# Performance work log

Hardware: AMD Instinct MI355X
Metric: run time of the kernel (lower is better)

Reference implementation:

```python
import jax, jax.numpy as jnp
import numpy as np
import math

D = 1024
H = 16
DH = D // H
B, M, N = 4, 1024, 2048
LN_EPS = 1e-5


def setup_inputs() -> dict:
    key = jax.random.key(0)
    ks = jax.random.split(key, 8)
    s = 1.0 / math.sqrt(D)  # keep logits well-scaled
    return {
        "Q": jax.random.normal(ks[0], (B, M, D), jnp.float32),
        "KV": jax.random.normal(ks[1], (B, N, D), jnp.float32),
        "log_gate_bias": jax.random.normal(ks[2], (B, N), jnp.float32),
        "Wq": jax.random.normal(ks[3], (D, D), jnp.float32) * s,
        "bq": jnp.zeros((D,), jnp.float32),
        "Wk": jax.random.normal(ks[4], (D, D), jnp.float32) * s,
        "bk": jnp.zeros((D,), jnp.float32),
        "Wv": jax.random.normal(ks[5], (D, D), jnp.float32) * s,
        "bv": jnp.zeros((D,), jnp.float32),
        "Wo": jax.random.normal(ks[6], (D, D), jnp.float32) * s,
        "bo": jnp.zeros((D,), jnp.float32),
        "gamma": jnp.ones((D,), jnp.float32),
        "beta": jnp.zeros((D,), jnp.float32),
    }


def reference(Q, KV, log_gate_bias, Wq, bq, Wk, bk, Wv, bv, Wo, bo, gamma, beta):
    b, m, d = Q.shape
    n = KV.shape[1]
    # projections (torch Linear: x @ W.T + b), split heads -> (b, h, len, dh)
    q = (Q @ Wq.T + bq).reshape(b, m, H, DH).transpose(0, 2, 1, 3)
    k = (KV @ Wk.T + bk).reshape(b, n, H, DH).transpose(0, 2, 1, 3)
    v = (KV @ Wv.T + bv).reshape(b, n, H, DH).transpose(0, 2, 1, 3)
    scores = jnp.einsum('bhmd,bhnd->bhmn', q, k) / math.sqrt(DH)
    # additive gate bias broadcast over heads and queries: (b,1,1,n)
    scores = scores + log_gate_bias[:, None, None, :]
    attn = jax.nn.softmax(scores, axis=-1)
    out = jnp.einsum('bhmn,bhnd->bhmd', attn, v)
    out = out.transpose(0, 2, 1, 3).reshape(b, m, d)
    out = out @ Wo.T + bo
    # dropout p=0.0 (eval) -> identity; residual + LayerNorm
    x = Q + out
    mu = jnp.mean(x, axis=-1, keepdims=True)
    var = jnp.mean(jnp.square(x - mu), axis=-1, keepdims=True)
    return gamma * (x - mu) * jax.lax.rsqrt(var + LN_EPS) + beta
```

## Files before the change

kernel.cpp:

```cpp
#include <hip/hip_runtime.h>
#include <hip/hip_bf16.h>

#define DMODEL 1024
#define NHEAD  16
#define DHEAD  64
#define BB     4
#define MM     1024
#define NN     2048
#define LOG2E  1.4426950408889634f

typedef __attribute__((ext_vector_type(8))) short bf16x8;
typedef __attribute__((ext_vector_type(4))) float f32x4;

#define AS1 __attribute__((address_space(1)))
#define AS3 __attribute__((address_space(3)))

__device__ __forceinline__ unsigned short f2bf(float f) {
  unsigned int u = __builtin_bit_cast(unsigned int, f);
  unsigned int r = (u + 0x7fffu + ((u >> 16) & 1u)) >> 16;
  return (unsigned short)r;
}

__global__ __launch_bounds__(256)
void cast_all(const float* __restrict__ Q, const float* __restrict__ KV,
              const float* __restrict__ W0, const float* __restrict__ W1,
              const float* __restrict__ W2, const float* __restrict__ W3,
              unsigned short* __restrict__ oQ, unsigned short* __restrict__ oKV,
              unsigned short* __restrict__ o0, unsigned short* __restrict__ o1,
              unsigned short* __restrict__ o2, unsigned short* __restrict__ o3)
{
  const int bid = blockIdx.x;
  const float* s; unsigned short* d; int i;
  if (bid < 4096)       { s = Q;  d = oQ;  i = bid * 256 + threadIdx.x; }
  else if (bid < 12288) { s = KV; d = oKV; i = (bid - 4096) * 256 + threadIdx.x; }
  else {
    const int w = (bid - 12288) >> 10;
    s = w == 0 ? W0 : w == 1 ? W1 : w == 2 ? W2 : W3;
    d = w == 0 ? o0 : w == 1 ? o1 : w == 2 ? o2 : o3;
    i = ((bid - 12288) & 1023) * 256 + threadIdx.x;
  }
  const float4 v = ((const float4*)s)[i];
  union { unsigned short us[4]; unsigned long long u64; } o;
  o.us[0] = f2bf(v.x); o.us[1] = f2bf(v.y); o.us[2] = f2bf(v.z); o.us[3] = f2bf(v.w);
  *(unsigned long long*)(d + (size_t)i * 4) = o.u64;
}

__global__ __launch_bounds__(256)
void qkv_gemm(const unsigned short* __restrict__ Qbf,
              const unsigned short* __restrict__ KVbf,
              const unsigned short* __restrict__ Wqb,
              const unsigned short* __restrict__ Wkb,
              const unsigned short* __restrict__ Wvb,
              const float* __restrict__ bq, const float* __restrict__ bk,
              const float* __restrict__ bv,
              unsigned short* __restrict__ qout,
              unsigned short* __restrict__ kout,
              unsigned short* __restrict__ vtout)
{
  __shared__ unsigned short As[3][128 * 32];
  __shared__ unsigned short Ws[3][128 * 32];

  const int bid = blockIdx.x;
  const unsigned short* A; const unsigned short* W; const float* bias;
  int mode, lb, nmb;
  if (bid < 256)      { A = Qbf;  W = Wqb; bias = bq; mode = 0; lb = bid;       nmb = 4; }
  else if (bid < 768) { A = KVbf; W = Wkb; bias = bk; mode = 1; lb = bid - 256; nmb = 8; }
  else                { A = KVbf; W = Wvb; bias = bv; mode = 2; lb = bid - 768; nmb = 8; }
  const int xcd = lb & 7;
  const int l   = lb >> 3;
  const int mb  = xcd * nmb + (l >> 3);
  const int nb  = l & 7;

  const int tid  = threadIdx.x;
  const int wave = tid >> 6;
  const int lane = tid & 63;
  const int l15  = lane & 15;
  const int l4   = lane >> 4;
  const int wm   = wave >> 1;
  const int wn   = wave & 1;
  const size_t row0 = (size_t)mb * 128;
  const size_t col0 = (size_t)nb * 128;

  f32x4 acc[4][4] = {};

  const int cc0 = (wave * 2) * 64 + lane;
  const int cc1 = cc0 + 64;
  const int r0 = cc0 >> 2, sch0 = (cc0 & 3) ^ (r0 & 3);
  const int r1 = cc1 >> 2, sch1 = (cc1 & 3) ^ (r1 & 3);
  const unsigned short* ap0 = A + (row0 + r0) * DMODEL + sch0 * 8;
  const unsigned short* ap1 = A + (row0 + r1) * DMODEL + sch1 * 8;
  const unsigned short* wp0 = W + (col0 + r0) * DMODEL + sch0 * 8;
  const unsigned short* wp1 = W + (col0 + r1) * DMODEL + sch1 * 8;

  auto stage = [&](int buf) {
    __builtin_amdgcn_global_load_lds((const AS1 void*)ap0, (AS3 void*)(&As[buf][cc0 * 8]), 16, 0, 0);
    __builtin_amdgcn_global_load_lds((const AS1 void*)ap1, (AS3 void*)(&As[buf][cc1 * 8]), 16, 0, 0);
    __builtin_amdgcn_global_load_lds((const AS1 void*)wp0, (AS3 void*)(&Ws[buf][cc0 * 8]), 16, 0, 0);
    __builtin_amdgcn_global_load_lds((const AS1 void*)wp1, (AS3 void*)(&Ws[buf][cc1 * 8]), 16, 0, 0);
    ap0 += 32; ap1 += 32; wp0 += 32; wp1 += 32;
  };

  stage(0);
  stage(1);

  int cur = 0;
  for (int kt = 0; kt < 32; ++kt) {
    if (kt < 31) {
      asm volatile("s_waitcnt vmcnt(4)" ::: "memory");
    } else {
      asm volatile("s_waitcnt vmcnt(0)" ::: "memory");
    }
    __builtin_amdgcn_sched_barrier(0);
    __builtin_amdgcn_s_barrier();
    __builtin_amdgcn_sched_barrier(0);
    if (kt < 30) {
      int nxt = cur + 2; if (nxt >= 3) nxt -= 3;
      stage(nxt);
    }

    bf16x8 af[4], bfr[4];
#pragma unroll
    for (int mi = 0; mi < 4; ++mi) {
      int r = wm * 64 + mi * 16 + l15;
      af[mi] = *(const bf16x8*)&As[cur][r * 32 + ((l4 ^ (r & 3)) << 3)];
    }
#pragma unroll
    for (int ni = 0; ni < 4; ++ni) {
      int r = wn * 64 + ni * 16 + l15;
      bfr[ni] = *(const bf16x8*)&Ws[cur][r * 32 + ((l4 ^ (r & 3)) << 3)];
    }
    __builtin_amdgcn_s_setprio(1);
#pragma unroll
    for (int mi = 0; mi < 4; ++mi)
#pragma unroll
      for (int ni = 0; ni < 4; ++ni)
        acc[mi][ni] = __builtin_amdgcn_mfma_f32_16x16x32_bf16(af[mi], bfr[ni], acc[mi][ni], 0, 0, 0);
    __builtin_amdgcn_s_setprio(0);

    cur = (cur == 2) ? 0 : cur + 1;
  }

#pragma unroll
  for (int mi = 0; mi < 4; ++mi) {
#pragma unroll
    for (int ni = 0; ni < 4; ++ni) {
      const int col = (int)col0 + wn * 64 + ni * 16 + l15;
      const float bcol = bias[col];
      if (mode == 2) {
        const int row = (int)row0 + wm * 64 + mi * 16 + l4 * 4;
        const int b = row >> 11, n = row & 2047;
        const int h = col >> 6, d = col & 63;
        union { unsigned short us[4]; uint2 u; } pk;
#pragma unroll
        for (int i = 0; i < 4; ++i)
          pk.us[i] = __builtin_bit_cast(unsigned short, __float2bfloat16(acc[mi][ni][i] + bcol));
        *(uint2*)(vtout + (((size_t)(b * 16 + h) * 64 + d) << 11) + n) = pk.u;
      } else {
#pragma unroll
        for (int i = 0; i < 4; ++i) {
          const size_t row = row0 + wm * 64 + mi * 16 + l4 * 4 + i;
          float v = acc[mi][ni][i] + bcol;
          if (mode == 0) v *= (0.125f * LOG2E);
          (mode == 0 ? qout : kout)[row * DMODEL + col] =
            __builtin_bit_cast(unsigned short, __float2bfloat16(v));
        }
      }
    }
  }
}

__global__ __launch_bounds__(256)
void gemm_o(const unsigned short* __restrict__ A,
            const unsigned short* __restrict__ W,
            const float* __restrict__ bias,
            const float* __restrict__ resid,
            float* __restrict__ out)
{
  __shared__ unsigned short As[3][64 * 32];
  __shared__ unsigned short Ws[3][128 * 32];

  const int bid = blockIdx.x;
  const int xcd = bid & 7;
  const int l   = bid >> 3;
  const int mb  = xcd * 8 + (l >> 3);
  const int nb  = l & 7;

  const int tid  = threadIdx.x;
  const int wave = tid >> 6;
  const int lane = tid & 63;
  const int l15  = lane & 15;
  const int l4   = lane >> 4;
  const int wm   = wave >> 1;
  const int wn   = wave & 1;
  const size_t row0 = (size_t)mb * 64;
  const size_t col0 = (size_t)nb * 128;

  f32x4 acc[2][4] = {};

  const int ra = tid >> 2, scha = (tid & 3) ^ (ra & 3);
  const int cc0 = (wave * 2) * 64 + lane;
  const int cc1 = cc0 + 64;
  const int r0 = cc0 >> 2, sch0 = (cc0 & 3) ^ (r0 & 3);
  const int r1 = cc1 >> 2, sch1 = (cc1 & 3) ^ (r1 & 3);
  const unsigned short* ap  = A + (row0 + ra) * DMODEL + scha * 8;
  const unsigned short* wp0 = W + (col0 + r0) * DMODEL + sch0 * 8;
  const unsigned short* wp1 = W + (col0 + r1) * DMODEL + sch1 * 8;

  auto stage = [&](int buf) {
    __builtin_amdgcn_global_load_lds((const AS1 void*)ap,  (AS3 void*)(&As[buf][tid * 8]), 16, 0, 0);
    __builtin_amdgcn_global_load_lds((const AS1 void*)wp0, (AS3 void*)(&Ws[buf][cc0 * 8]), 16, 0, 0);
    __builtin_amdgcn_global_load_lds((const AS1 void*)wp1, (AS3 void*)(&Ws[buf][cc1 * 8]), 16, 0, 0);
    ap += 32; wp0 += 32; wp1 += 32;
  };

  stage(0);
  stage(1);

  int cur = 0;
  for (int kt = 0; kt < 32; ++kt) {
    if (kt < 31) {
      asm volatile("s_waitcnt vmcnt(3)" ::: "memory");
    } else {
      asm volatile("s_waitcnt vmcnt(0)" ::: "memory");
    }
    __builtin_amdgcn_sched_barrier(0);
    __builtin_amdgcn_s_barrier();
    __builtin_amdgcn_sched_barrier(0);
    if (kt < 30) {
      int nxt = cur + 2; if (nxt >= 3) nxt -= 3;
      stage(nxt);
    }

    bf16x8 af[2], bfr[4];
#pragma unroll
    for (int mi = 0; mi < 2; ++mi) {
      int r = wm * 32 + mi * 16 + l15;
      af[mi] = *(const bf16x8*)&As[cur][r * 32 + ((l4 ^ (r & 3)) << 3)];
    }
#pragma unroll
    for (int ni = 0; ni < 4; ++ni) {
      int r = wn * 64 + ni * 16 + l15;
      bfr[ni] = *(const bf16x8*)&Ws[cur][r * 32 + ((l4 ^ (r & 3)) << 3)];
    }
    __builtin_amdgcn_s_setprio(1);
#pragma unroll
    for (int mi = 0; mi < 2; ++mi)
#pragma unroll
      for (int ni = 0; ni < 4; ++ni)
        acc[mi][ni] = __builtin_amdgcn_mfma_f32_16x16x32_bf16(af[mi], bfr[ni], acc[mi][ni], 0, 0, 0);
    __builtin_amdgcn_s_setprio(0);

    cur = (cur == 2) ? 0 : cur + 1;
  }

#pragma unroll
  for (int mi = 0; mi < 2; ++mi) {
#pragma unroll
    for (int ni = 0; ni < 4; ++ni) {
      const int col = (int)col0 + wn * 64 + ni * 16 + l15;
      const float bcol = bias[col];
#pragma unroll
      for (int i = 0; i < 4; ++i) {
        const size_t row = row0 + wm * 32 + mi * 16 + l4 * 4 + i;
        const size_t idx = row * DMODEL + col;
        out[idx] = resid[idx] + acc[mi][ni][i] + bcol;
      }
    }
  }
}

__global__ __launch_bounds__(512, 4)
void attn_kernel(const unsigned short* __restrict__ qb,
                 const unsigned short* __restrict__ kb,
                 const unsigned short* __restrict__ vt,
                 const float* __restrict__ lgb,
                 unsigned short* __restrict__ attn)
{
  __shared__ unsigned short Ks[2][64 * 64];
  __shared__ unsigned short Vs[2][64 * 64];
  __shared__ float Gs[2][64];
  __shared__ unsigned short Ps[8][16 * 64];

  const int tid  = threadIdx.x;
  const int wave = tid >> 6;
  const int lane = tid & 63;
  const int l15  = lane & 15;
  const int l4   = lane >> 4;

  const int bid  = blockIdx.x;
  const int xcd  = bid & 7;
  const int slot = bid >> 3;
  const int m_i  = slot & 7;
  const int grp  = slot >> 3;
  const int bh   = grp * 8 + xcd;
  const int b    = bh >> 4;
  const int h    = bh & 15;
  const int m0   = m_i * 128;

  const unsigned short* qg = qb + ((size_t)(b * MM + m0)) * DMODEL + h * DHEAD;
  const unsigned short* kg = kb + ((size_t)b * NN) * DMODEL + h * DHEAD;
  const unsigned short* vg = vt + ((size_t)(b * NHEAD + h)) * (DHEAD * (size_t)NN);

  bf16x8 qf0, qf1;
  {
    const unsigned short* qrow = qg + (size_t)(wave * 16 + l15) * DMODEL;
    qf0 = *(const bf16x8*)(qrow + l4 * 8);
    qf1 = *(const bf16x8*)(qrow + 32 + l4 * 8);
  }

  bf16x8 ones;
  {
    const short one = (l15 == 0) ? (short)0x3f80 : (short)0;
#pragma unroll
    for (int j = 0; j < 8; ++j) ones[j] = one;
  }

  const int sr = tid >> 3;
  const int sc = (tid & 7) ^ (sr & 7);
  const unsigned short* kp = kg + (size_t)sr * DMODEL + (sc << 3);
  const unsigned short* vp = vg + (size_t)sr * NN + (sc << 3);
  const float* gp = lgb + (size_t)b * NN + lane;

  auto stage = [&](int buf) {
    if (wave == 0)
      __builtin_amdgcn_global_load_lds((const AS1 void*)gp, (AS3 void*)(&Gs[buf][lane]), 4, 0, 0);
    __builtin_amdgcn_global_load_lds((const AS1 void*)kp, (AS3 void*)(&Ks[buf][tid * 8]), 16, 0, 0);
    __builtin_amdgcn_global_load_lds((const AS1 void*)vp, (AS3 void*)(&Vs[buf][tid * 8]), 16, 0, 0);
    kp += 64 * DMODEL; vp += 64; gp += 64;
  };

  stage(0);

  f32x4 ovec[5] = {};
  unsigned short* Pw = &Ps[wave][0];
  const int pbase = l15 * 128;
  const int s7 = l15 & 7;

  for (int nt = 0; nt < NN / 64; ++nt) {
    const int cur = nt & 1;
    asm volatile("s_waitcnt vmcnt(0)" ::: "memory");
    __builtin_amdgcn_sched_barrier(0);
    __builtin_amdgcn_s_barrier();
    __builtin_amdgcn_sched_barrier(0);
    if (nt < NN / 64 - 1) stage(cur ^ 1);

    f32x4 s[4];
    __builtin_amdgcn_s_setprio(1);
#pragma unroll
    for (int ni = 0; ni < 4; ++ni) {
      const int r = ni * 16 + l15;
      const int c0 = l4 ^ (r & 7);
      bf16x8 kf0 = *(const bf16x8*)&Ks[cur][r * 64 + (c0 << 3)];
      bf16x8 kf1 = *(const bf16x8*)&Ks[cur][r * 64 + ((c0 ^ 4) << 3)];
      f32x4 z = {};
      z = __builtin_amdgcn_mfma_f32_16x16x32_bf16(kf0, qf0, z, 0, 0, 0);
      s[ni] = __builtin_amdgcn_mfma_f32_16x16x32_bf16(kf1, qf1, z, 0, 0, 0);
    }
    __builtin_amdgcn_s_setprio(0);

#pragma unroll
    for (int ni = 0; ni < 4; ++ni) {
      const float4 g = *(const float4*)&Gs[cur][ni * 16 + l4 * 4];
      union { unsigned short us[4]; uint2 u; } pk;
      pk.us[0] = __builtin_bit_cast(unsigned short,
                   __float2bfloat16(__builtin_amdgcn_exp2f(fmaf(g.x, LOG2E, s[ni][0]))));
      pk.us[1] = __builtin_bit_cast(unsigned short,
                   __float2bfloat16(__builtin_amdgcn_exp2f(fmaf(g.y, LOG2E, s[ni][1]))));
      pk.us[2] = __builtin_bit_cast(unsigned short,
                   __float2bfloat16(__builtin_amdgcn_exp2f(fmaf(g.z, LOG2E, s[ni][2]))));
      pk.us[3] = __builtin_bit_cast(unsigned short,
                   __float2bfloat16(__builtin_amdgcn_exp2f(fmaf(g.w, LOG2E, s[ni][3]))));
      *(uint2*)((char*)Pw + pbase + (((ni * 4 + l4) ^ (s7 << 1)) << 3)) = pk.u;
    }
    asm volatile("s_waitcnt lgkmcnt(0)" ::: "memory");
    __builtin_amdgcn_sched_barrier(0);

    __builtin_amdgcn_s_setprio(1);
#pragma unroll
    for (int ks2 = 0; ks2 < 2; ++ks2) {
      const bf16x8 pf = *(const bf16x8*)((const char*)Pw + pbase + (((ks2 * 4 + l4) ^ s7) << 4));
#pragma unroll
      for (int di = 0; di < 4; ++di) {
        const int d = di * 16 + l15;
        const bf16x8 vf = *(const bf16x8*)&Vs[cur][d * 64 + (((ks2 * 4 + l4) ^ (d & 7)) << 3)];
        ovec[di] = __builtin_amdgcn_mfma_f32_16x16x32_bf16(pf, vf, ovec[di], 0, 0, 0);
      }
      ovec[4] = __builtin_amdgcn_mfma_f32_16x16x32_bf16(pf, ones, ovec[4], 0, 0, 0);
    }
    __builtin_amdgcn_s_setprio(0);
  }

  const int lsrc = lane & 48;
  float linv[4];
#pragma unroll
  for (int i = 0; i < 4; ++i)
    linv[i] = 1.0f / __shfl(ovec[4][i], lsrc);
#pragma unroll
  for (int di = 0; di < 4; ++di)
#pragma unroll
    for (int i = 0; i < 4; ++i) {
      const int row = m0 + wave * 16 + l4 * 4 + i;
      const int col = h * DHEAD + di * 16 + l15;
      attn[((size_t)(b * MM + row)) * DMODEL + col] =
        __builtin_bit_cast(unsigned short, __float2bfloat16(ovec[di][i] * linv[i]));
    }
}

__global__ __launch_bounds__(256)
void ln_kernel(const float* __restrict__ x, const float* __restrict__ gamma,
               const float* __restrict__ beta, float* __restrict__ out)
{
  __shared__ float sh1[4], sh2[4];
  const int t = threadIdx.x;
  const size_t row = blockIdx.x;
  const float4 v = ((const float4*)(x + row * DMODEL))[t];

  float s = v.x + v.y + v.z + v.w;
#pragma unroll
  for (int m = 1; m < 64; m <<= 1) s += __shfl_xor(s, m);
  if ((t & 63) == 0) sh1[t >> 6] = s;
  __syncthreads();
  const float mu = (sh1[0] + sh1[1] + sh1[2] + sh1[3]) * (1.0f / DMODEL);

  const float dx = v.x - mu, dy = v.y - mu, dz = v.z - mu, dw = v.w - mu;
  float q = dx * dx + dy * dy + dz * dz + dw * dw;
#pragma unroll
  for (int m = 1; m < 64; m <<= 1) q += __shfl_xor(q, m);
  if ((t & 63) == 0) sh2[t >> 6] = q;
  __syncthreads();
  const float var = (sh2[0] + sh2[1] + sh2[2] + sh2[3]) * (1.0f / DMODEL);
  const float rstd = rsqrtf(var + 1e-5f);

  const float4 g  = ((const float4*)gamma)[t];
  const float4 be = ((const float4*)beta)[t];
  float4 o;
  o.x = dx * rstd * g.x + be.x;
  o.y = dy * rstd * g.y + be.y;
  o.z = dz * rstd * g.z + be.z;
  o.w = dw * rstd * g.w + be.w;
  ((float4*)(out + row * DMODEL))[t] = o;
}

extern "C" void kernel_launch(void* const* d_in, const int* in_sizes, int n_in,
                              void* d_out, int out_size, void* d_ws, size_t ws_size,
                              hipStream_t stream)
{
  const float* Qf    = (const float*)d_in[0];
  const float* KVf   = (const float*)d_in[1];
  const float* lgb   = (const float*)d_in[2];
  const float* Wq    = (const float*)d_in[3];
  const float* bq    = (const float*)d_in[4];
  const float* Wk    = (const float*)d_in[5];
  const float* bk    = (const float*)d_in[6];
  const float* Wv    = (const float*)d_in[7];
  const float* bv    = (const float*)d_in[8];
  const float* Wo    = (const float*)d_in[9];
  const float* bo    = (const float*)d_in[10];
  const float* gamma = (const float*)d_in[11];
  const float* beta  = (const float*)d_in[12];
  float* out = (float*)d_out;

  char* ws = (char*)d_ws;
  unsigned short* Qbf   = (unsigned short*)(ws + 0);
  unsigned short* attnb = Qbf;
  unsigned short* KVbf  = (unsigned short*)(ws + 8388608);
  float*          xbuf  = (float*)(ws + 8388608);
  unsigned short* Wqb = (unsigned short*)(ws + 25165824);
  unsigned short* Wkb = (unsigned short*)(ws + 27262976);
  unsigned short* Wvb = (unsigned short*)(ws + 29360128);
  unsigned short* Wob = (unsigned short*)(ws + 31457280);
  unsigned short* qbuf  = (unsigned short*)(ws + 33554432);
  unsigned short* kbuf  = (unsigned short*)(ws + 41943040);
  unsigned short* vtbuf = (unsigned short*)(ws + 58720256);

  cast_all<<<16384, dim3(256), 0, stream>>>(Qf, KVf, Wq, Wk, Wv, Wo,
                                            Qbf, KVbf, Wqb, Wkb, Wvb, Wob);

  qkv_gemm<<<1280, dim3(256), 0, stream>>>(Qbf, KVbf, Wqb, Wkb, Wvb,
                                           bq, bk, bv, qbuf, kbuf, vtbuf);

  attn_kernel<<<512, dim3(512), 0, stream>>>(qbuf, kbuf, vtbuf, lgb, attnb);

  gemm_o<<<512, dim3(256), 0, stream>>>(attnb, Wob, bo, Qf, xbuf);

  ln_kernel<<<4096, dim3(256), 0, stream>>>(xbuf, gamma, beta, out);
}
```

Measured before the change: 153.5 us.

## Fuse fp32-to-bf16 activation cast into QKV GEMM register-staged A loads

Removes the activation cast pass for Q and KV, so the separate kernel now casts only the weights. The QKV GEMM reads fp32 activations directly into registers, converts them to bf16 and writes them into a double-buffered LDS tile, while weights still use direct global-to-LDS loads with triple buffering. This saves a full read/write round trip of the activations in bf16. In exchange, the GEMM reads twice the A bytes per tile, and KV is re-read by both the K and V blocks. The register staging also adds VGPR pressure and conversion ALU work inside the main loop.

```diff
diff --git a/kernel.cpp b/kernel.cpp
--- a/kernel.cpp
+++ b/kernel.cpp
@@ -21,24 +21,25 @@
   return (unsigned short)r;
 }
 
+__device__ __forceinline__ bf16x8 cvt8(float4 lo, float4 hi) {
+  bf16x8 r;
+  r[0] = (short)f2bf(lo.x); r[1] = (short)f2bf(lo.y);
+  r[2] = (short)f2bf(lo.z); r[3] = (short)f2bf(lo.w);
+  r[4] = (short)f2bf(hi.x); r[5] = (short)f2bf(hi.y);
+  r[6] = (short)f2bf(hi.z); r[7] = (short)f2bf(hi.w);
+  return r;
+}
+
 __global__ __launch_bounds__(256)
-void cast_all(const float* __restrict__ Q, const float* __restrict__ KV,
-              const float* __restrict__ W0, const float* __restrict__ W1,
-              const float* __restrict__ W2, const float* __restrict__ W3,
-              unsigned short* __restrict__ oQ, unsigned short* __restrict__ oKV,
-              unsigned short* __restrict__ o0, unsigned short* __restrict__ o1,
-              unsigned short* __restrict__ o2, unsigned short* __restrict__ o3)
+void cast_w(const float* __restrict__ W0, const float* __restrict__ W1,
+            const float* __restrict__ W2, const float* __restrict__ W3,
+            unsigned short* __restrict__ o0, unsigned short* __restrict__ o1,
+            unsigned short* __restrict__ o2, unsigned short* __restrict__ o3)
 {
-  const int bid = blockIdx.x;
-  const float* s; unsigned short* d; int i;
-  if (bid < 4096)       { s = Q;  d = oQ;  i = bid * 256 + threadIdx.x; }
-  else if (bid < 12288) { s = KV; d = oKV; i = (bid - 4096) * 256 + threadIdx.x; }
-  else {
-    const int w = (bid - 12288) >> 10;
-    s = w == 0 ? W0 : w == 1 ? W1 : w == 2 ? W2 : W3;
-    d = w == 0 ? o0 : w == 1 ? o1 : w == 2 ? o2 : o3;
-    i = ((bid - 12288) & 1023) * 256 + threadIdx.x;
-  }
+  const int w = blockIdx.x >> 10;
+  const float* s = w == 0 ? W0 : w == 1 ? W1 : w == 2 ? W2 : W3;
+  unsigned short* d = w == 0 ? o0 : w == 1 ? o1 : w == 2 ? o2 : o3;
+  const int i = (blockIdx.x & 1023) * 256 + threadIdx.x;
   const float4 v = ((const float4*)s)[i];
   union { unsigned short us[4]; unsigned long long u64; } o;
   o.us[0] = f2bf(v.x); o.us[1] = f2bf(v.y); o.us[2] = f2bf(v.z); o.us[3] = f2bf(v.w);
@@ -46,8 +47,8 @@
 }
 
 __global__ __launch_bounds__(256)
-void qkv_gemm(const unsigned short* __restrict__ Qbf,
-              const unsigned short* __restrict__ KVbf,
+void qkv_gemm(const float* __restrict__ Qf,
+              const float* __restrict__ KVf,
               const unsigned short* __restrict__ Wqb,
               const unsigned short* __restrict__ Wkb,
               const unsigned short* __restrict__ Wvb,
@@ -57,15 +58,15 @@
               unsigned short* __restrict__ kout,
               unsigned short* __restrict__ vtout)
 {
-  __shared__ unsigned short As[3][128 * 32];
+  __shared__ unsigned short As[2][128 * 32];
   __shared__ unsigned short Ws[3][128 * 32];
 
   const int bid = blockIdx.x;
-  const unsigned short* A; const unsigned short* W; const float* bias;
+  const float* A; const unsigned short* W; const float* bias;
   int mode, lb, nmb;
-  if (bid < 256)      { A = Qbf;  W = Wqb; bias = bq; mode = 0; lb = bid;       nmb = 4; }
-  else if (bid < 768) { A = KVbf; W = Wkb; bias = bk; mode = 1; lb = bid - 256; nmb = 8; }
-  else                { A = KVbf; W = Wvb; bias = bv; mode = 2; lb = bid - 768; nmb = 8; }
+  if (bid < 256)      { A = Qf;  W = Wqb; bias = bq; mode = 0; lb = bid;       nmb = 4; }
+  else if (bid < 768) { A = KVf; W = Wkb; bias = bk; mode = 1; lb = bid - 256; nmb = 8; }
+  else                { A = KVf; W = Wvb; bias = bv; mode = 2; lb = bid - 768; nmb = 8; }
   const int xcd = lb & 7;
   const int l   = lb >> 3;
   const int mb  = xcd * nmb + (l >> 3);
@@ -87,47 +88,63 @@
   const int cc1 = cc0 + 64;
   const int r0 = cc0 >> 2, sch0 = (cc0 & 3) ^ (r0 & 3);
   const int r1 = cc1 >> 2, sch1 = (cc1 & 3) ^ (r1 & 3);
-  const unsigned short* ap0 = A + (row0 + r0) * DMODEL + sch0 * 8;
-  const unsigned short* ap1 = A + (row0 + r1) * DMODEL + sch1 * 8;
+  const float* a0p = A + (row0 + r0) * DMODEL + sch0 * 8;
+  const float* a1p = A + (row0 + r1) * DMODEL + sch1 * 8;
   const unsigned short* wp0 = W + (col0 + r0) * DMODEL + sch0 * 8;
   const unsigned short* wp1 = W + (col0 + r1) * DMODEL + sch1 * 8;
 
-  auto stage = [&](int buf) {
-    __builtin_amdgcn_global_load_lds((const AS1 void*)ap0, (AS3 void*)(&As[buf][cc0 * 8]), 16, 0, 0);
-    __builtin_amdgcn_global_load_lds((const AS1 void*)ap1, (AS3 void*)(&As[buf][cc1 * 8]), 16, 0, 0);
-    __builtin_amdgcn_global_load_lds((const AS1 void*)wp0, (AS3 void*)(&Ws[buf][cc0 * 8]), 16, 0, 0);
-    __builtin_amdgcn_global_load_lds((const AS1 void*)wp1, (AS3 void*)(&Ws[buf][cc1 * 8]), 16, 0, 0);
-    ap0 += 32; ap1 += 32; wp0 += 32; wp1 += 32;
+  float4 a0lo, a0hi, a1lo, a1hi;
+
+  auto loadA = [&]() {
+    a0lo = *(const float4*)a0p; a0hi = *(const float4*)(a0p + 4);
+    a1lo = *(const float4*)a1p; a1hi = *(const float4*)(a1p + 4);
+    a0p += 32; a1p += 32;
   };
-
-  stage(0);
-  stage(1);
-
-  int cur = 0;
+  auto writeA = [&](int slot) {
+    *(bf16x8*)&As[slot][cc0 * 8] = cvt8(a0lo, a0hi);
+    *(bf16x8*)&As[slot][cc1 * 8] = cvt8(a1lo, a1hi);
+  };
+  auto stageW = [&](int slot) {
+    __builtin_amdgcn_global_load_lds((const AS1 void*)wp0, (AS3 void*)(&Ws[slot][cc0 * 8]), 16, 0, 0);
+    __builtin_amdgcn_global_load_lds((const AS1 void*)wp1, (AS3 void*)(&Ws[slot][cc1 * 8]), 16, 0, 0);
+    wp0 += 32; wp1 += 32;
+  };
+
+  loadA();
+  stageW(0);
+  writeA(0);
+  loadA();
+  stageW(1);
+  asm volatile("s_waitcnt lgkmcnt(0)" ::: "memory");
+
+  int curW = 0;
   for (int kt = 0; kt < 32; ++kt) {
     if (kt < 31) {
-      asm volatile("s_waitcnt vmcnt(4)" ::: "memory");
+      asm volatile("s_waitcnt vmcnt(6)" ::: "memory");
     } else {
       asm volatile("s_waitcnt vmcnt(0)" ::: "memory");
     }
     __builtin_amdgcn_sched_barrier(0);
     __builtin_amdgcn_s_barrier();
     __builtin_amdgcn_sched_barrier(0);
+
+    if (kt < 31) writeA((kt + 1) & 1);
     if (kt < 30) {
-      int nxt = cur + 2; if (nxt >= 3) nxt -= 3;
-      stage(nxt);
+      loadA();
+      int nxt = curW + 2; if (nxt >= 3) nxt -= 3;
+      stageW(nxt);
     }
 
     bf16x8 af[4], bfr[4];
 #pragma unroll
     for (int mi = 0; mi < 4; ++mi) {
       int r = wm * 64 + mi * 16 + l15;
-      af[mi] = *(const bf16x8*)&As[cur][r * 32 + ((l4 ^ (r & 3)) << 3)];
+      af[mi] = *(const bf16x8*)&As[kt & 1][r * 32 + ((l4 ^ (r & 3)) << 3)];
     }
 #pragma unroll
     for (int ni = 0; ni < 4; ++ni) {
       int r = wn * 64 + ni * 16 + l15;
-      bfr[ni] = *(const bf16x8*)&Ws[cur][r * 32 + ((l4 ^ (r & 3)) << 3)];
+      bfr[ni] = *(const bf16x8*)&Ws[curW][r * 32 + ((l4 ^ (r & 3)) << 3)];
     }
     __builtin_amdgcn_s_setprio(1);
 #pragma unroll
@@ -137,7 +154,7 @@
         acc[mi][ni] = __builtin_amdgcn_mfma_f32_16x16x32_bf16(af[mi], bfr[ni], acc[mi][ni], 0, 0, 0);
     __builtin_amdgcn_s_setprio(0);
 
-    cur = (cur == 2) ? 0 : cur + 1;
+    curW = (curW == 2) ? 0 : curW + 1;
   }
 
 #pragma unroll
@@ -461,9 +478,7 @@
   float* out = (float*)d_out;
 
   char* ws = (char*)d_ws;
-  unsigned short* Qbf   = (unsigned short*)(ws + 0);
-  unsigned short* attnb = Qbf;
-  unsigned short* KVbf  = (unsigned short*)(ws + 8388608);
+  unsigned short* attnb = (unsigned short*)(ws + 0);
   float*          xbuf  = (float*)(ws + 8388608);
   unsigned short* Wqb = (unsigned short*)(ws + 25165824);
   unsigned short* Wkb = (unsigned short*)(ws + 27262976);
@@ -473,10 +488,9 @@
   unsigned short* kbuf  = (unsigned short*)(ws + 41943040);
   unsigned short* vtbuf = (unsigned short*)(ws + 58720256);
 
-  cast_all<<<16384, dim3(256), 0, stream>>>(Qf, KVf, Wq, Wk, Wv, Wo,
-                                            Qbf, KVbf, Wqb, Wkb, Wvb, Wob);
-
-  qkv_gemm<<<1280, dim3(256), 0, stream>>>(Qbf, KVbf, Wqb, Wkb, Wvb,
+  cast_w<<<4096, dim3(256), 0, stream>>>(Wq, Wk, Wv, Wo, Wqb, Wkb, Wvb, Wob);
+
+  qkv_gemm<<<1280, dim3(256), 0, stream>>>(Qf, KVf, Wqb, Wkb, Wvb,
                                            bq, bk, bv, qbuf, kbuf, vtbuf);
 
   attn_kernel<<<512, dim3(512), 0, stream>>>(qbuf, kbuf, vtbuf, lgb, attnb);
```

New measurement: 154.5 us. About the same (+0.6%).
